# Kernel tuning notes

Measured on AMD Instinct MI355X. Metric: run time of the kernel, lower is better.

Reference implementation:

```python
import jax, jax.numpy as jnp
import numpy as np

D = 1024      # d_model
H = 16        # num_heads
DK = D // H   # head dim
L = 6         # num_layers
DFF = 4 * D   # feed-forward width
V = 32000     # vocab
B = 8         # batch
TP1 = 513     # target tokens (x length); decoded length = 512
S = 1024      # encoder frames
MAXLEN = 512
EPS = 1e-6


def make_pe(max_len, d):
    pos = np.arange(max_len, dtype=np.float64)[:, None]
    i = np.arange(0, d, 2, dtype=np.float64)[None, :]
    ang = pos / np.power(10000.0, i / d)
    pe = np.zeros((max_len, d), dtype=np.float32)
    pe[:, 0::2] = np.sin(ang)
    pe[:, 1::2] = np.cos(ang)
    return jnp.asarray(pe)


def setup_inputs() -> dict:
    key = jax.random.key(0)
    ks = jax.random.split(key, 16)
    sc = 0.02
    inp = {
        'x': jax.random.randint(ks[0], (B, TP1), 0, V, dtype=jnp.int64),
        'encoder_output': jax.random.normal(ks[1], (B, S, D), jnp.float32),
        'emb': jax.random.normal(ks[2], (V, D), jnp.float32) * sc,
        'pe': make_pe(MAXLEN, D),
        # per-layer stacked params; index 0..3 = q,k,v,out projections (in,out layout)
        'attn1_w': jax.random.normal(ks[3], (L, 4, D, D), jnp.float32) * sc,
        'attn1_b': jnp.zeros((L, 4, D), jnp.float32),
        'attn2_w': jax.random.normal(ks[4], (L, 4, D, D), jnp.float32) * sc,
        'attn2_b': jnp.zeros((L, 4, D), jnp.float32),
        'norm_a': jnp.ones((L, 3, D), jnp.float32),
        'norm_b': jnp.zeros((L, 3, D), jnp.float32),
        'ff1_w': jax.random.normal(ks[5], (L, D, DFF), jnp.float32) * sc,
        'ff1_b': jnp.zeros((L, DFF), jnp.float32),
        'ff2_w': jax.random.normal(ks[6], (L, DFF, D), jnp.float32) * sc,
        'ff2_b': jnp.zeros((L, D), jnp.float32),
        'fc_w': jax.random.normal(ks[7], (D, V), jnp.float32) * sc,
        'fc_b': jnp.zeros((V,), jnp.float32),
    }
    return inp


def _norm(x, a, b):
    mu = jnp.mean(x, axis=-1, keepdims=True)
    # torch .std() default is unbiased (ddof=1)
    var = jnp.sum((x - mu) ** 2, axis=-1, keepdims=True) / (x.shape[-1] - 1)
    return a * (x - mu) / (jnp.sqrt(var) + EPS) + b


def _mha(q_in, kv_in, w, b):
    # w: [4, D, D], b: [4, D]; masks in the original are no-ops (bug), omitted.
    bs, tq, _ = q_in.shape
    q = (q_in @ w[0] + b[0]).reshape(bs, tq, H, DK).transpose(0, 2, 1, 3)
    k = (kv_in @ w[1] + b[1]).reshape(bs, -1, H, DK).transpose(0, 2, 1, 3)
    v = (kv_in @ w[2] + b[2]).reshape(bs, -1, H, DK).transpose(0, 2, 1, 3)
    score = jnp.einsum('bhqd,bhkd->bhqk', q, k) / np.sqrt(DK).astype(np.float32)
    attn = jax.nn.softmax(score, axis=-1)
    o = jnp.einsum('bhqk,bhkd->bhqd', attn, v)
    o = o.transpose(0, 2, 1, 3).reshape(bs, tq, D)
    return o @ w[3] + b[3]


def reference(x, encoder_output, emb, pe, attn1_w, attn1_b, attn2_w, attn2_b,
              norm_a, norm_b, ff1_w, ff1_b, ff2_w, ff2_b, fc_w, fc_b):
    t = x.shape[1] - 1
    h = emb[x[:, :-1]] + pe[None, :t, :]  # [B, T, D]
    for l in range(L):
        a1 = _mha(h, h, attn1_w[l], attn1_b[l])
        h = _norm(a1 + h, norm_a[l, 0], norm_b[l, 0])
        a2 = _mha(h, encoder_output, attn2_w[l], attn2_b[l])
        h = _norm(a2 + h, norm_a[l, 1], norm_b[l, 1])
        f = jax.nn.relu(h @ ff1_w[l] + ff1_b[l]) @ ff2_w[l] + ff2_b[l]
        h = _norm(f + h, norm_a[l, 2], norm_b[l, 2])
    logits = h @ fc_w + fc_b  # [B, T, V]
    return jax.nn.log_softmax(logits, axis=-1)
```

## Files before the change

### kernel.cpp

```cpp
#include <hip/hip_runtime.h>

typedef __attribute__((ext_vector_type(4))) float f32x4;
typedef __attribute__((ext_vector_type(8))) __bf16 bfx8;
typedef unsigned short u16;
typedef unsigned int u32;

__device__ __forceinline__ u16 f2bf(float f) {
  u32 u = __builtin_bit_cast(u32, f);
  u = (u + 0x7FFFu + ((u >> 16) & 1u)) >> 16;
  return (u16)u;
}
__device__ __forceinline__ float bf2f(u16 u) {
  return __builtin_bit_cast(float, ((u32)u) << 16);
}

typedef __attribute__((address_space(1))) const void gvoid;
typedef __attribute__((address_space(3))) void svoid;
__device__ __forceinline__ void gload16(const void* g, void* l) {
  __builtin_amdgcn_global_load_lds((gvoid*)g, (svoid*)l, 16, 0, 0);
}

__device__ __forceinline__ float wredsum(float v) {
#pragma unroll
  for (int o = 32; o; o >>= 1) v += __shfl_xor(v, o, 64);
  return v;
}
__device__ __forceinline__ float wredmax(float v) {
#pragma unroll
  for (int o = 32; o; o >>= 1) v = fmaxf(v, __shfl_xor(v, o, 64));
  return v;
}

__global__ __launch_bounds__(256) void wconv_kernel(const float* __restrict__ in,
                                                    u16* __restrict__ out, int K, int N) {
  __shared__ u16 tile[32][33];
  const long z = blockIdx.z;
  const float* iz = in + z * (long)K * N;
  u16* oz = out + z * (long)K * N;
  const int n0 = blockIdx.x << 5, k0 = blockIdx.y << 5;
  const int tx = threadIdx.x & 31, ty = threadIdx.x >> 5;
#pragma unroll
  for (int i = 0; i < 4; ++i)
    tile[ty + 8 * i][tx] = f2bf(iz[(long)(k0 + ty + 8 * i) * N + n0 + tx]);
  __syncthreads();
#pragma unroll
  for (int i = 0; i < 4; ++i)
    oz[(long)(n0 + ty + 8 * i) * K + k0 + tx] = tile[tx][ty + 8 * i];
}

__global__ __launch_bounds__(256) void cvt_kernel(const float* __restrict__ in,
                                                  u16* __restrict__ out, long n) {
  long i = ((long)blockIdx.x * 256 + threadIdx.x) * 4;
  if (i + 3 < n) {
    float4 v = *(const float4*)(in + i);
    ushort4 o = {f2bf(v.x), f2bf(v.y), f2bf(v.z), f2bf(v.w)};
    *(ushort4*)(out + i) = o;
  }
}

__global__ __launch_bounds__(256) void embed_kernel(const int* __restrict__ x,
                                                    const float* __restrict__ emb,
                                                    const float* __restrict__ pe,
                                                    float* __restrict__ h,
                                                    u16* __restrict__ hb) {
  const int row = blockIdx.x;
  const int b = row >> 9, t = row & 511;
  const long tok = (long)x[b * 513 + t];
  const int d = threadIdx.x << 2;
  float4 e = *(const float4*)(emb + tok * 1024 + d);
  float4 p = *(const float4*)(pe + (long)t * 1024 + d);
  float4 v = {e.x + p.x, e.y + p.y, e.z + p.z, e.w + p.w};
  *(float4*)(h + (long)row * 1024 + d) = v;
  ushort4 o = {f2bf(v.x), f2bf(v.y), f2bf(v.z), f2bf(v.w)};
  *(ushort4*)(hb + (long)row * 1024 + d) = o;
}

__global__ __launch_bounds__(256) void addnorm_kernel(const float* __restrict__ delta,
                                                      const float* __restrict__ delta2,
                                                      float* __restrict__ h,
                                                      u16* __restrict__ hb,
                                                      const float* __restrict__ ga,
                                                      const float* __restrict__ gb) {
  __shared__ float r1[4], r2[4];
  const long row = blockIdx.x;
  const int d = threadIdx.x << 2;
  float4 a = *(const float4*)(h + row * 1024 + d);
  float4 q = *(const float4*)(delta + row * 1024 + d);
  float4 q2 = *(const float4*)(delta2 + row * 1024 + d);
  float x0 = a.x + q.x + q2.x, x1 = a.y + q.y + q2.y;
  float x2 = a.z + q.z + q2.z, x3 = a.w + q.w + q2.w;
  float s1 = wredsum(x0 + x1 + x2 + x3);
  float s2 = wredsum(x0 * x0 + x1 * x1 + x2 * x2 + x3 * x3);
  if ((threadIdx.x & 63) == 0) { r1[threadIdx.x >> 6] = s1; r2[threadIdx.x >> 6] = s2; }
  __syncthreads();
  float S1 = r1[0] + r1[1] + r1[2] + r1[3];
  float S2 = r2[0] + r2[1] + r2[2] + r2[3];
  float mu = S1 * (1.0f / 1024.0f);
  float var = (S2 - S1 * mu) * (1.0f / 1023.0f);
  float inv = 1.0f / (sqrtf(fmaxf(var, 0.f)) + 1e-6f);
  float4 g4 = *(const float4*)(ga + d);
  float4 b4 = *(const float4*)(gb + d);
  float y0 = g4.x * (x0 - mu) * inv + b4.x;
  float y1 = g4.y * (x1 - mu) * inv + b4.y;
  float y2 = g4.z * (x2 - mu) * inv + b4.z;
  float y3 = g4.w * (x3 - mu) * inv + b4.w;
  float4 y = {y0, y1, y2, y3};
  *(float4*)(h + row * 1024 + d) = y;
  ushort4 o = {f2bf(y0), f2bf(y1), f2bf(y2), f2bf(y3)};
  *(ushort4*)(hb + row * 1024 + d) = o;
}

__global__ __launch_bounds__(256) void logsoftmax_kernel(float* __restrict__ lg) {
  const long row = blockIdx.x;
  float* lr = lg + row * 32000L;
  float m = -1e30f, s = 0.f;
  for (int j = threadIdx.x; j < 8000; j += 256) {
    float4 v = *(const float4*)(lr + (long)j * 4);
    float lm = fmaxf(fmaxf(v.x, v.y), fmaxf(v.z, v.w));
    if (lm > m) { s *= __expf(m - lm); m = lm; }
    s += __expf(v.x - m) + __expf(v.y - m) + __expf(v.z - m) + __expf(v.w - m);
  }
#pragma unroll
  for (int o = 32; o; o >>= 1) {
    float om = __shfl_xor(m, o, 64), os = __shfl_xor(s, o, 64);
    float M = fmaxf(m, om);
    s = s * __expf(m - M) + os * __expf(om - M);
    m = M;
  }
  __shared__ float rm[4], rs[4];
  if ((threadIdx.x & 63) == 0) { rm[threadIdx.x >> 6] = m; rs[threadIdx.x >> 6] = s; }
  __syncthreads();
  float M = fmaxf(fmaxf(rm[0], rm[1]), fmaxf(rm[2], rm[3]));
  float S = rs[0] * __expf(rm[0] - M) + rs[1] * __expf(rm[1] - M) +
            rs[2] * __expf(rm[2] - M) + rs[3] * __expf(rm[3] - M);
  float lse = M + __logf(S);
  for (int j = threadIdx.x; j < 8000; j += 256) {
    float4 v = *(const float4*)(lr + (long)j * 4);
    v.x -= lse; v.y -= lse; v.z -= lse; v.w -= lse;
    *(float4*)(lr + (long)j * 4) = v;
  }
}

__global__ __launch_bounds__(512) void logsoftmax_bf16_kernel(const u16* __restrict__ lg,
                                                              float* __restrict__ out) {
  __shared__ u16 rl[32000];
  __shared__ float rr[8];
  const long row = blockIdx.x;
  const u16* lr = lg + row * 32000L;
  float* od = out + row * 32000L;
  const int tid = threadIdx.x;
  float m0 = -1e30f, m1 = -1e30f;
  for (int j = tid * 8; j < 32000; j += 4096) {
    ushort4 a = *(const ushort4*)(lr + j);
    ushort4 b = *(const ushort4*)(lr + j + 4);
    *(ushort4*)&rl[j] = a;
    *(ushort4*)&rl[j + 4] = b;
    m0 = fmaxf(m0, fmaxf(fmaxf(bf2f(a.x), bf2f(a.y)), fmaxf(bf2f(a.z), bf2f(a.w))));
    m1 = fmaxf(m1, fmaxf(fmaxf(bf2f(b.x), bf2f(b.y)), fmaxf(bf2f(b.z), bf2f(b.w))));
  }
  float m = wredmax(fmaxf(m0, m1));
  if ((tid & 63) == 0) rr[tid >> 6] = m;
  __syncthreads();
  m = fmaxf(fmaxf(fmaxf(rr[0], rr[1]), fmaxf(rr[2], rr[3])),
            fmaxf(fmaxf(rr[4], rr[5]), fmaxf(rr[6], rr[7])));
  __syncthreads();
  float s0 = 0.f, s1 = 0.f;
  for (int j = tid * 8; j < 32000; j += 4096) {
    ushort4 a = *(const ushort4*)&rl[j];
    ushort4 b = *(const ushort4*)&rl[j + 4];
    s0 += __expf(bf2f(a.x) - m) + __expf(bf2f(a.y) - m) +
          __expf(bf2f(a.z) - m) + __expf(bf2f(a.w) - m);
    s1 += __expf(bf2f(b.x) - m) + __expf(bf2f(b.y) - m) +
          __expf(bf2f(b.z) - m) + __expf(bf2f(b.w) - m);
  }
  float s = wredsum(s0 + s1);
  if ((tid & 63) == 0) rr[tid >> 6] = s;
  __syncthreads();
  s = rr[0] + rr[1] + rr[2] + rr[3] + rr[4] + rr[5] + rr[6] + rr[7];
  const float lse = m + __logf(s);
  for (int j = tid * 8; j < 32000; j += 4096) {
    ushort4 a = *(const ushort4*)&rl[j];
    ushort4 b = *(const ushort4*)&rl[j + 4];
    float4 o0 = {bf2f(a.x) - lse, bf2f(a.y) - lse, bf2f(a.z) - lse, bf2f(a.w) - lse};
    float4 o1 = {bf2f(b.x) - lse, bf2f(b.y) - lse, bf2f(b.z) - lse, bf2f(b.w) - lse};
    *(float4*)(od + j) = o0;
    *(float4*)(od + j + 4) = o1;
  }
}

template <int SKV>
__global__ __launch_bounds__(512) void attn_kernel(const u16* __restrict__ Q,
                                                   const u16* __restrict__ Kb,
                                                   const u16* __restrict__ Vt,
                                                   u16* __restrict__ ctx) {
  __shared__ u16 Kl[2][4096];
  __shared__ u16 Vl[2][4096];
  __shared__ u16 Pl[8][16][72];
  const int tid = threadIdx.x, lane = tid & 63, wave = tid >> 6;
  const int l15 = lane & 15, lg = lane >> 4;
  const int bh = blockIdx.y;
  const int qrow = blockIdx.x * 128 + wave * 16 + l15;
  const u16* qp = Q + ((long)bh * 512 + qrow) * 64 + lg * 8;
  bfx8 qf0 = *(const bfx8*)(qp);
  bfx8 qf1 = *(const bfx8*)(qp + 32);

  const int srow = tid >> 3;
  const int schunk = (tid & 7) ^ (srow & 7);
  const u16* Kbb = Kb + ((long)bh * SKV + srow) * 64 + schunk * 8;
  const u16* Vtb2 = Vt + ((long)bh * 64 + srow) * SKV + schunk * 8;

  auto stage = [&](int t, int buf) {
    const int kv0 = t * 64;
    gload16(Kbb + (long)kv0 * 64, &Kl[buf][tid * 8]);
    gload16(Vtb2 + kv0, &Vl[buf][tid * 8]);
  };

  const f32x4 zf = {0.f, 0.f, 0.f, 0.f};
  f32x4 acc_o[4] = {zf, zf, zf, zf};
  float mrun = -1e30f, lrun = 0.f;
  const int swk = l15 & 7;
  constexpr int NT = SKV / 64;

  stage(0, 0);
  __syncthreads();
  int buf = 0;
#pragma unroll 1
  for (int t = 0; t < NT; ++t) {
    if (t + 1 < NT) stage(t + 1, buf ^ 1);
    f32x4 sacc[4];
    __builtin_amdgcn_s_setprio(1);
#pragma unroll
    for (int kvt = 0; kvt < 4; ++kvt) {
      const int krow = kvt * 16 + l15;
      bfx8 kf0 = *(const bfx8*)&Kl[buf][krow * 64 + ((lg ^ swk) << 3)];
      bfx8 kf1 = *(const bfx8*)&Kl[buf][krow * 64 + (((4 + lg) ^ swk) << 3)];
      f32x4 tt = __builtin_amdgcn_mfma_f32_16x16x32_bf16(kf0, qf0, zf, 0, 0, 0);
      sacc[kvt] = __builtin_amdgcn_mfma_f32_16x16x32_bf16(kf1, qf1, tt, 0, 0, 0);
    }
    __builtin_amdgcn_s_setprio(0);
    float pm = -1e30f;
#pragma unroll
    for (int kvt = 0; kvt < 4; ++kvt)
#pragma unroll
      for (int r = 0; r < 4; ++r) pm = fmaxf(pm, sacc[kvt][r]);
    pm = fmaxf(pm, __shfl_xor(pm, 16, 64));
    pm = fmaxf(pm, __shfl_xor(pm, 32, 64));
    pm *= 0.125f;
    const bool grow = !__all(pm <= mrun);
    const float mnew = grow ? fmaxf(mrun, pm) : mrun;
    float psum = 0.f;
#pragma unroll
    for (int kvt = 0; kvt < 4; ++kvt)
#pragma unroll
      for (int r = 0; r < 4; ++r) {
        float p = __expf(sacc[kvt][r] * 0.125f - mnew);
        psum += p;
        Pl[wave][l15][kvt * 16 + lg * 4 + r] = f2bf(p);
      }
    psum += __shfl_xor(psum, 16, 64);
    psum += __shfl_xor(psum, 32, 64);
    if (grow) {
      const float corr = __expf(mrun - mnew);
      lrun = lrun * corr + psum;
      mrun = mnew;
#pragma unroll
      for (int dt = 0; dt < 4; ++dt) {
        acc_o[dt][0] *= corr; acc_o[dt][1] *= corr;
        acc_o[dt][2] *= corr; acc_o[dt][3] *= corr;
      }
    } else {
      lrun += psum;
    }
    bfx8 pf0 = *(const bfx8*)&Pl[wave][l15][lg * 8];
    bfx8 pf1 = *(const bfx8*)&Pl[wave][l15][32 + lg * 8];
    __builtin_amdgcn_s_setprio(1);
#pragma unroll
    for (int dt = 0; dt < 4; ++dt) {
      const int vrow = dt * 16 + l15;
      bfx8 vf0 = *(const bfx8*)&Vl[buf][vrow * 64 + ((lg ^ swk) << 3)];
      bfx8 vf1 = *(const bfx8*)&Vl[buf][vrow * 64 + (((4 + lg) ^ swk) << 3)];
      acc_o[dt] = __builtin_amdgcn_mfma_f32_16x16x32_bf16(vf0, pf0, acc_o[dt], 0, 0, 0);
      acc_o[dt] = __builtin_amdgcn_mfma_f32_16x16x32_bf16(vf1, pf1, acc_o[dt], 0, 0, 0);
    }
    __builtin_amdgcn_s_setprio(0);
    __syncthreads();
    buf ^= 1;
  }
  const float inv = 1.0f / lrun;
  const int b = bh >> 4, hh = bh & 15;
  u16* crow = ctx + ((long)b * 512 + qrow) * 1024 + hh * 64;
#pragma unroll
  for (int dt = 0; dt < 4; ++dt)
#pragma unroll
    for (int r = 0; r < 4; ++r)
      crow[dt * 16 + lg * 4 + r] = f2bf(acc_o[dt][r] * inv);
}

template <int BM, int BN, int WMW, int WNW, int EPI, bool RELU>
__global__ __launch_bounds__(256) void gemm_bt(const u16* __restrict__ A, long sAz, int lda,
                                               const u16* __restrict__ Bt, long sBz, int ldb,
                                               const float* __restrict__ bias,
                                               void* __restrict__ out, long sCz, int ldc,
                                               int K, int Ttok) {
  constexpr int WROWS = BM / WMW, WCOLS = BN / WNW;
  constexpr int MI = WROWS / 16, NI = WCOLS / 16;
  __shared__ u16 As[BM * 32];
  __shared__ u16 Bs[BN * 32];
  const int tid = threadIdx.x, lane = tid & 63, wave = tid >> 6;
  const int l15 = lane & 15, lg = lane >> 4;
  const int wm = wave / WNW, wn = wave % WNW;
  const int bx = blockIdx.x, by = blockIdx.y;
  const long z = blockIdx.z;
  const int srow = tid >> 2, scol = (tid & 3) << 3;
  const u16* Aa = A + z * sAz + (long)(by * BM + srow) * lda + scol;
  const u16* Ba = Bt + z * sBz + (long)(bx * BN + srow) * ldb + scol;

  f32x4 acc[MI][NI];
#pragma unroll
  for (int i = 0; i < MI; ++i)
#pragma unroll
    for (int j = 0; j < NI; ++j) acc[i][j] = (f32x4){0.f, 0.f, 0.f, 0.f};

  for (int kt = 0; kt < K; kt += 32) {
#pragma unroll
    for (int i = 0; i < BM / 64; ++i)
      gload16(Aa + (long)i * 64 * lda + kt, &As[i * 2048 + tid * 8]);
#pragma unroll
    for (int i = 0; i < BN / 64; ++i)
      gload16(Ba + (long)i * 64 * ldb + kt, &Bs[i * 2048 + tid * 8]);
    __syncthreads();
    bfx8 afr[MI], bfr[NI];
#pragma unroll
    for (int i = 0; i < MI; ++i)
      afr[i] = *(const bfx8*)&As[(wm * WROWS + i * 16 + l15) * 32 + (lg << 3)];
#pragma unroll
    for (int j = 0; j < NI; ++j)
      bfr[j] = *(const bfx8*)&Bs[(wn * WCOLS + j * 16 + l15) * 32 + (lg << 3)];
#pragma unroll
    for (int i = 0; i < MI; ++i)
#pragma unroll
      for (int j = 0; j < NI; ++j)
        acc[i][j] = __builtin_amdgcn_mfma_f32_16x16x32_bf16(afr[i], bfr[j], acc[i][j], 0, 0, 0);
    __syncthreads();
  }

  const int gm0 = by * BM + wm * WROWS;
  const int gn0 = bx * BN + wn * WCOLS;
#pragma unroll
  for (int i = 0; i < MI; ++i) {
#pragma unroll
    for (int j = 0; j < NI; ++j) {
      const int gn = gn0 + j * 16 + l15;
      const float bv = (bias && z == 0) ? bias[gn] : 0.f;
#pragma unroll
      for (int r = 0; r < 4; ++r) {
        const int gm = gm0 + i * 16 + (lg << 2) + r;
        float v = acc[i][j][r] + bv;
        if (RELU) v = fmaxf(v, 0.f);
        if constexpr (EPI == 0) {
          ((float*)out)[z * sCz + (long)gm * ldc + gn] = v;
        } else if constexpr (EPI == 1) {
          ((u16*)out)[z * sCz + (long)gm * ldc + gn] = f2bf(v);
        } else if constexpr (EPI == 3) {
          const int b = gm / Ttok, t = gm - b * Ttok;
          const int hh = gn >> 6, dk = gn & 63;
          ((u16*)out)[(((long)(b * 16 + hh) * Ttok + t) << 6) + dk] = f2bf(v);
        }
      }
    }
  }
}

#define MMAQ(hm, hn)                                                                   \
  {                                                                                    \
    _Pragma("unroll") for (int kk = 0; kk < 2; ++kk)                                   \
        _Pragma("unroll") for (int i = 0; i < 4; ++i)                                  \
            _Pragma("unroll") for (int jn = 0; jn < 2; ++jn)                           \
                acc[(hm)*4 + i][(hn)*2 + jn] = __builtin_amdgcn_mfma_f32_16x16x32_bf16( \
                    a[i][kk], b[jn][kk], acc[(hm)*4 + i][(hn)*2 + jn], 0, 0, 0);       \
  }

template <int EPI, bool RELU, int BMAP>
__global__ __launch_bounds__(512, 2) void gemm256(const u16* __restrict__ A, int lda,
                                                  const u16* __restrict__ Bt, int ldb,
                                                  const float* __restrict__ bias,
                                                  void* __restrict__ out, int ldc, int K,
                                                  int Ttok, void* __restrict__ out2,
                                                  void* __restrict__ out3, int gx) {
  __shared__ u16 lds[2][2][2][8192];
  const int tid = threadIdx.x, lane = tid & 63;
  const int wid = tid >> 6, wm = wid >> 2, wn = wid & 3;
  const int l15 = lane & 15, lg = lane >> 4;
  const int S = gx >> 3;
  const int xcd = blockIdx.x & 7, idx = blockIdx.x >> 3;
  const int mt = xcd * S + idx % S;
  const int nt_ = idx / S;
  const int NT = K >> 6;

  const int r0 = tid >> 3;
  const int blkx = (tid & 7) ^ (r0 & 7);
  const int n0 = nt_ * 256;
  long brow0;
  if constexpr (BMAP == 1)
    brow0 = (long)(n0 >> 11) * 4096 + 1024 + (n0 & 2047);
  else
    brow0 = n0;
  const u16* Abase = A + (long)(mt * 256 + r0) * lda + blkx * 8;
  const u16* Bbase = Bt + (brow0 + r0) * ldb + blkx * 8;

  auto stageA = [&](int s, int half) {
    const int kts = (s < NT ? s : NT - 1) << 6;
    const u16* g = Abase + (long)(half * 128) * lda + kts;
    gload16(g, &lds[s & 1][0][half][tid * 8]);
    gload16(g + (long)64 * lda, &lds[s & 1][0][half][(512 + tid) * 8]);
  };
  auto stageB = [&](int s, int half) {
    const int kts = (s < NT ? s : NT - 1) << 6;
    const u16* g = Bbase + (long)(half * 128) * ldb + kts;
    gload16(g, &lds[s & 1][1][half][tid * 8]);
    gload16(g + (long)64 * ldb, &lds[s & 1][1][half][(512 + tid) * 8]);
  };

  f32x4 acc[8][4];
#pragma unroll
  for (int i = 0; i < 8; ++i)
#pragma unroll
    for (int j = 0; j < 4; ++j) acc[i][j] = (f32x4){0.f, 0.f, 0.f, 0.f};
  bfx8 a[4][2], b[2][2];

  const int sw = l15 & 7;
  auto loadA = [&](int buf, int hm) {
#pragma unroll
    for (int i = 0; i < 4; ++i) {
      const int row = hm * 64 + i * 16 + l15;
#pragma unroll
      for (int kk = 0; kk < 2; ++kk)
        a[i][kk] = *(const bfx8*)&lds[buf][0][wm][row * 64 + (((kk * 4 + lg) ^ sw) << 3)];
    }
  };
  auto loadB = [&](int buf, int hn) {
#pragma unroll
    for (int jn = 0; jn < 2; ++jn) {
      const int row = (wn & 1) * 64 + hn * 32 + jn * 16 + l15;
#pragma unroll
      for (int kk = 0; kk < 2; ++kk)
        b[jn][kk] = *(const bfx8*)&lds[buf][1][wn >> 1][row * 64 + (((kk * 4 + lg) ^ sw) << 3)];
    }
  };

  stageA(0, 0); stageA(0, 1); stageB(0, 0); stageB(0, 1);
  stageA(1, 0); stageA(1, 1);
  asm volatile("s_waitcnt vmcnt(4)" ::: "memory");
  __builtin_amdgcn_s_barrier();

  for (int t = 0; t < NT; ++t) {
    const int p = t & 1;
    loadA(p, 0); loadB(p, 0);
    stageB(t + 1, 0);
    __builtin_amdgcn_s_barrier();
    asm volatile("s_waitcnt lgkmcnt(0)" ::: "memory");
    __builtin_amdgcn_s_setprio(1);
    MMAQ(0, 0);
    __builtin_amdgcn_s_setprio(0);
    __builtin_amdgcn_s_barrier();
    loadB(p, 1);
    stageB(t + 1, 1);
    __builtin_amdgcn_s_barrier();
    asm volatile("s_waitcnt lgkmcnt(0)" ::: "memory");
    __builtin_amdgcn_s_setprio(1);
    MMAQ(0, 1);
    __builtin_amdgcn_s_setprio(0);
    __builtin_amdgcn_s_barrier();
    loadA(p, 1); loadB(p, 0);
    stageA(t + 2, 0);
    __builtin_amdgcn_s_barrier();
    asm volatile("s_waitcnt lgkmcnt(0)" ::: "memory");
    __builtin_amdgcn_s_setprio(1);
    MMAQ(1, 0);
    __builtin_amdgcn_s_setprio(0);
    __builtin_amdgcn_s_barrier();
    loadB(p, 1);
    stageA(t + 2, 1);
    asm volatile("s_waitcnt vmcnt(4)" ::: "memory");
    __builtin_amdgcn_s_barrier();
    asm volatile("s_waitcnt lgkmcnt(0)" ::: "memory");
    __builtin_amdgcn_s_setprio(1);
    MMAQ(1, 1);
    __builtin_amdgcn_s_setprio(0);
    __builtin_amdgcn_s_barrier();
  }

  const int gm0 = mt * 256 + wm * 128;
  const int gn0 = nt_ * 256 + wn * 64;
#pragma unroll
  for (int ii = 0; ii < 8; ++ii) {
#pragma unroll
    for (int jj = 0; jj < 4; ++jj) {
      const int gn = gn0 + jj * 16 + l15;
      float bv;
      if constexpr (BMAP == 1)
        bv = bias[(gn >> 11) * 4096 + 1024 + (gn & 2047)];
      else
        bv = bias ? bias[gn] : 0.f;
#pragma unroll
      for (int r = 0; r < 4; ++r) {
        const int gm = gm0 + ii * 16 + (lg << 2) + r;
        float v = acc[ii][jj][r] + bv;
        if (RELU) v = fmaxf(v, 0.f);
        if constexpr (EPI == 0) {
          ((float*)out)[(long)gm * ldc + gn] = v;
        } else if constexpr (EPI == 1) {
          ((u16*)out)[(long)gm * ldc + gn] = f2bf(v);
        } else if constexpr (EPI == 6) {
          const int bq = gm / Ttok, t2 = gm - bq * Ttok;
          const int sec = gn >> 10, w1 = gn & 1023;
          const int hh = w1 >> 6, dk = w1 & 63;
          const u16 val = f2bf(v);
          if (sec == 0)
            ((u16*)out)[(((long)(bq * 16 + hh) * Ttok + t2) << 6) + dk] = val;
          else if (sec == 1)
            ((u16*)out2)[(((long)(bq * 16 + hh) * Ttok + t2) << 6) + dk] = val;
          else
            ((u16*)out3)[((long)((bq * 16 + hh) << 6) + dk) * Ttok + t2] = val;
        } else if constexpr (EPI == 7) {
          const int bq = gm / Ttok, t2 = gm - bq * Ttok;
          const int sec = gn >> 10, w1 = gn & 1023;
          const int hh = w1 >> 6, dk = w1 & 63;
          const u16 val = f2bf(v);
          if (sec == 0)
            ((u16*)out)[(((long)(bq * 16 + hh) * Ttok + t2) << 6) + dk] = val;
          else
            ((u16*)out2)[((long)((bq * 16 + hh) << 6) + dk) * Ttok + t2] = val;
        } else if constexpr (EPI == 8) {
          const int l = gn >> 11, inner = gn & 2047;
          const int sec = inner >> 10, w1 = inner & 1023;
          const int hh = w1 >> 6, dk = w1 & 63;
          const int bq = gm >> 10, t2 = gm & 1023;
          const u16 val = f2bf(v);
          if (sec == 0)
            ((u16*)out)[((((long)l * 8 + bq) * 16 + hh) * 1024 + t2) * 64 + dk] = val;
          else
            ((u16*)out2)[((((long)l * 8 + bq) * 16 + hh) * 64 + dk) * 1024 + t2] = val;
        }
      }
    }
  }
}

extern "C" void kernel_launch(void* const* d_in, const int* in_sizes, int n_in,
                              void* d_out, int out_size, void* d_ws, size_t ws_size,
                              hipStream_t stream) {
  const int* x = (const int*)d_in[0];
  const float* enc = (const float*)d_in[1];
  const float* emb = (const float*)d_in[2];
  const float* pe = (const float*)d_in[3];
  const float* a1w = (const float*)d_in[4];
  const float* a1b = (const float*)d_in[5];
  const float* a2w = (const float*)d_in[6];
  const float* a2b = (const float*)d_in[7];
  const float* nra = (const float*)d_in[8];
  const float* nrb = (const float*)d_in[9];
  const float* f1w = (const float*)d_in[10];
  const float* f1b = (const float*)d_in[11];
  const float* f2w = (const float*)d_in[12];
  const float* f2b = (const float*)d_in[13];
  const float* fcw = (const float*)d_in[14];
  const float* fcb = (const float*)d_in[15];
  float* out = (float*)d_out;

  char* base = (char*)d_ws;
  size_t off = 0;
  auto alloc = [&](size_t bytes) -> void* {
    void* p = base + off;
    off += (bytes + 255) & ~(size_t)255;
    return p;
  };
  const long wsz = 1024 * 1024;
  const bool big = ws_size >= (600ull << 20);
  u16* wT = (u16*)alloc(96ull * wsz * 2);
  u16* encb = (u16*)alloc(8ull * wsz * 2);
  float* h = (float*)alloc(4ull * wsz * 4);
  u16* hb = (u16*)alloc(4ull * wsz * 2);
  u16* qb = (u16*)alloc(4ull * wsz * 2);
  u16* kb = (u16*)alloc(8ull * wsz * 2);
  u16* vtb = (u16*)alloc(8ull * wsz * 2);
  u16* ctxb = (u16*)alloc(4ull * wsz * 2);
  float* af = (float*)alloc(4ull * wsz * 4);
  float* af2 = (float*)alloc(4ull * wsz * 4);
  u16* midb = (u16*)alloc(16ull * wsz * 2);
  u16* fcT = qb;
  u16* kv6 = big ? (u16*)alloc(262144000) : nullptr;
  u16* kb6 = kv6;
  u16* vtb6 = kv6 ? kv6 + 50331648 : nullptr;
  u16* lgb = kv6;

  u16* wTa1 = wT;
  u16* wTa2 = wT + 24 * wsz;
  u16* wTf1 = wT + 48 * wsz;
  u16* wTf2 = wT + 72 * wsz;

  cvt_kernel<<<dim3(8192), dim3(256), 0, stream>>>(enc, encb, 8ll * wsz);
  embed_kernel<<<dim3(4096), dim3(256), 0, stream>>>(x, emb, pe, h, hb);
  wconv_kernel<<<dim3(32, 32, 24), dim3(256), 0, stream>>>(a1w, wTa1, 1024, 1024);
  wconv_kernel<<<dim3(32, 32, 24), dim3(256), 0, stream>>>(a2w, wTa2, 1024, 1024);
  wconv_kernel<<<dim3(128, 32, 6), dim3(256), 0, stream>>>(f1w, wTf1, 1024, 4096);
  wconv_kernel<<<dim3(32, 128, 6), dim3(256), 0, stream>>>(f2w, wTf2, 4096, 1024);

  if (big) {
    gemm256<8, false, 1><<<dim3(1536), dim3(512), 0, stream>>>(
        encb, 1024, wTa2, 1024, a2b, kb6, 0, 1024, 1024, vtb6, nullptr, 32);
  }

  for (int l = 0; l < 6; ++l) {
    const float* b1 = a1b + (long)l * 4096;
    const float* b2 = a2b + (long)l * 4096;
    const u16* w1 = wTa1 + (long)l * 4 * wsz;
    const u16* w2 = wTa2 + (long)l * 4 * wsz;

    gemm256<6, false, 0><<<dim3(192), dim3(512), 0, stream>>>(
        hb, 1024, w1, 1024, b1, qb, 0, 1024, 512, kb, vtb, 16);
    attn_kernel<512><<<dim3(4, 128), dim3(512), 0, stream>>>(qb, kb, vtb, ctxb);
    gemm_bt<128, 128, 2, 2, 0, false><<<dim3(8, 32, 2), dim3(256), 0, stream>>>(
        ctxb, 512, 1024, w1 + 3 * wsz, 512, 1024, b1 + 3072, af, 4194304, 1024, 512, 0);
    addnorm_kernel<<<dim3(4096), dim3(256), 0, stream>>>(
        af, af2, h, hb, nra + (l * 3 + 0) * 1024, nrb + (l * 3 + 0) * 1024);

    gemm_bt<64, 128, 2, 2, 3, false><<<dim3(8, 64, 1), dim3(256), 0, stream>>>(
        hb, 0, 1024, w2, 0, 1024, b2, qb, 0, 0, 1024, 512);
    const u16* lK;
    const u16* lV;
    if (big) {
      lK = kb6 + (long)l * 8388608;
      lV = vtb6 + (long)l * 8388608;
    } else {
      gemm256<7, false, 0><<<dim3(256), dim3(512), 0, stream>>>(
          encb, 1024, w2 + wsz, 1024, b2 + 1024, kb, 0, 1024, 1024, vtb, nullptr, 32);
      lK = kb;
      lV = vtb;
    }
    attn_kernel<1024><<<dim3(4, 128), dim3(512), 0, stream>>>(qb, lK, lV, ctxb);
    gemm_bt<128, 128, 2, 2, 0, false><<<dim3(8, 32, 2), dim3(256), 0, stream>>>(
        ctxb, 512, 1024, w2 + 3 * wsz, 512, 1024, b2 + 3072, af, 4194304, 1024, 512, 0);
    addnorm_kernel<<<dim3(4096), dim3(256), 0, stream>>>(
        af, af2, h, hb, nra + (l * 3 + 1) * 1024, nrb + (l * 3 + 1) * 1024);

    gemm256<1, true, 0><<<dim3(256), dim3(512), 0, stream>>>(
        hb, 1024, wTf1 + (long)l * 4 * wsz, 1024, f1b + (long)l * 4096, midb, 4096, 1024, 0,
        nullptr, nullptr, 16);
    gemm_bt<128, 128, 2, 2, 0, false><<<dim3(8, 32, 2), dim3(256), 0, stream>>>(
        midb, 2048, 4096, wTf2 + (long)l * 4 * wsz, 2048, 4096, f2b + (long)l * 1024, af,
        4194304, 1024, 2048, 0);
    addnorm_kernel<<<dim3(4096), dim3(256), 0, stream>>>(
        af, af2, h, hb, nra + (l * 3 + 2) * 1024, nrb + (l * 3 + 2) * 1024);
  }

  wconv_kernel<<<dim3(1000, 32, 1), dim3(256), 0, stream>>>(fcw, fcT, 1024, 32000);
  if (big) {
    gemm256<1, false, 0><<<dim3(2000), dim3(512), 0, stream>>>(
        hb, 1024, fcT, 1024, fcb, lgb, 32000, 1024, 0, nullptr, nullptr, 16);
    logsoftmax_bf16_kernel<<<dim3(4096), dim3(512), 0, stream>>>(lgb, out);
  } else {
    gemm256<0, false, 0><<<dim3(2000), dim3(512), 0, stream>>>(
        hb, 1024, fcT, 1024, fcb, out, 32000, 1024, 0, nullptr, nullptr, 16);
    logsoftmax_kernel<<<dim3(4096), dim3(256), 0, stream>>>(out);
  }
}
```

Measured before the change: 3.031 ms.

## Store split-K partials in bf16 and split FF2 GEMM four ways

Split-K partial outputs of the output-projection and FF2 GEMMs are now written as bf16 (epilogue mode 1) into a single partial buffer instead of two fp32 buffers. The add-norm kernel is templated on the number of partials and sums them in fp32. FF2 goes from a 2-way to a 4-way K split, which raises grid parallelism. This halves the partial-sum memory traffic but rounds the partials to bf16, and the 4-way split adds one more partial read per row.

```diff
diff --git a/kernel.cpp b/kernel.cpp
--- a/kernel.cpp
+++ b/kernel.cpp
@@ -75,8 +75,8 @@
   *(ushort4*)(hb + (long)row * 1024 + d) = o;
 }
 
-__global__ __launch_bounds__(256) void addnorm_kernel(const float* __restrict__ delta,
-                                                      const float* __restrict__ delta2,
+template <int NP>
+__global__ __launch_bounds__(256) void addnorm_kernel(const u16* __restrict__ pb,
                                                       float* __restrict__ h,
                                                       u16* __restrict__ hb,
                                                       const float* __restrict__ ga,
@@ -85,10 +85,12 @@
   const long row = blockIdx.x;
   const int d = threadIdx.x << 2;
   float4 a = *(const float4*)(h + row * 1024 + d);
-  float4 q = *(const float4*)(delta + row * 1024 + d);
-  float4 q2 = *(const float4*)(delta2 + row * 1024 + d);
-  float x0 = a.x + q.x + q2.x, x1 = a.y + q.y + q2.y;
-  float x2 = a.z + q.z + q2.z, x3 = a.w + q.w + q2.w;
+  float x0 = a.x, x1 = a.y, x2 = a.z, x3 = a.w;
+#pragma unroll
+  for (int n = 0; n < NP; ++n) {
+    ushort4 q = *(const ushort4*)(pb + (long)n * 4194304 + row * 1024 + d);
+    x0 += bf2f(q.x); x1 += bf2f(q.y); x2 += bf2f(q.z); x3 += bf2f(q.w);
+  }
   float s1 = wredsum(x0 + x1 + x2 + x3);
   float s2 = wredsum(x0 * x0 + x1 * x1 + x2 * x2 + x3 * x3);
   if ((threadIdx.x & 63) == 0) { r1[threadIdx.x >> 6] = s1; r2[threadIdx.x >> 6] = s2; }
@@ -585,8 +587,7 @@
   u16* kb = (u16*)alloc(8ull * wsz * 2);
   u16* vtb = (u16*)alloc(8ull * wsz * 2);
   u16* ctxb = (u16*)alloc(4ull * wsz * 2);
-  float* af = (float*)alloc(4ull * wsz * 4);
-  float* af2 = (float*)alloc(4ull * wsz * 4);
+  u16* pb = (u16*)alloc(16ull * wsz * 2);
   u16* midb = (u16*)alloc(16ull * wsz * 2);
   u16* fcT = qb;
   u16* kv6 = big ? (u16*)alloc(262144000) : nullptr;
@@ -620,10 +621,10 @@
     gemm256<6, false, 0><<<dim3(192), dim3(512), 0, stream>>>(
         hb, 1024, w1, 1024, b1, qb, 0, 1024, 512, kb, vtb, 16);
     attn_kernel<512><<<dim3(4, 128), dim3(512), 0, stream>>>(qb, kb, vtb, ctxb);
-    gemm_bt<128, 128, 2, 2, 0, false><<<dim3(8, 32, 2), dim3(256), 0, stream>>>(
-        ctxb, 512, 1024, w1 + 3 * wsz, 512, 1024, b1 + 3072, af, 4194304, 1024, 512, 0);
-    addnorm_kernel<<<dim3(4096), dim3(256), 0, stream>>>(
-        af, af2, h, hb, nra + (l * 3 + 0) * 1024, nrb + (l * 3 + 0) * 1024);
+    gemm_bt<128, 128, 2, 2, 1, false><<<dim3(8, 32, 2), dim3(256), 0, stream>>>(
+        ctxb, 512, 1024, w1 + 3 * wsz, 512, 1024, b1 + 3072, pb, 4194304, 1024, 512, 0);
+    addnorm_kernel<2><<<dim3(4096), dim3(256), 0, stream>>>(
+        pb, h, hb, nra + (l * 3 + 0) * 1024, nrb + (l * 3 + 0) * 1024);
 
     gemm_bt<64, 128, 2, 2, 3, false><<<dim3(8, 64, 1), dim3(256), 0, stream>>>(
         hb, 0, 1024, w2, 0, 1024, b2, qb, 0, 0, 1024, 512);
@@ -639,19 +640,19 @@
       lV = vtb;
     }
     attn_kernel<1024><<<dim3(4, 128), dim3(512), 0, stream>>>(qb, lK, lV, ctxb);
-    gemm_bt<128, 128, 2, 2, 0, false><<<dim3(8, 32, 2), dim3(256), 0, stream>>>(
-        ctxb, 512, 1024, w2 + 3 * wsz, 512, 1024, b2 + 3072, af, 4194304, 1024, 512, 0);
-    addnorm_kernel<<<dim3(4096), dim3(256), 0, stream>>>(
-        af, af2, h, hb, nra + (l * 3 + 1) * 1024, nrb + (l * 3 + 1) * 1024);
+    gemm_bt<128, 128, 2, 2, 1, false><<<dim3(8, 32, 2), dim3(256), 0, stream>>>(
+        ctxb, 512, 1024, w2 + 3 * wsz, 512, 1024, b2 + 3072, pb, 4194304, 1024, 512, 0);
+    addnorm_kernel<2><<<dim3(4096), dim3(256), 0, stream>>>(
+        pb, h, hb, nra + (l * 3 + 1) * 1024, nrb + (l * 3 + 1) * 1024);
 
     gemm256<1, true, 0><<<dim3(256), dim3(512), 0, stream>>>(
         hb, 1024, wTf1 + (long)l * 4 * wsz, 1024, f1b + (long)l * 4096, midb, 4096, 1024, 0,
         nullptr, nullptr, 16);
-    gemm_bt<128, 128, 2, 2, 0, false><<<dim3(8, 32, 2), dim3(256), 0, stream>>>(
-        midb, 2048, 4096, wTf2 + (long)l * 4 * wsz, 2048, 4096, f2b + (long)l * 1024, af,
-        4194304, 1024, 2048, 0);
-    addnorm_kernel<<<dim3(4096), dim3(256), 0, stream>>>(
-        af, af2, h, hb, nra + (l * 3 + 2) * 1024, nrb + (l * 3 + 2) * 1024);
+    gemm_bt<128, 128, 2, 2, 1, false><<<dim3(8, 32, 4), dim3(256), 0, stream>>>(
+        midb, 1024, 4096, wTf2 + (long)l * 4 * wsz, 1024, 4096, f2b + (long)l * 1024, pb,
+        4194304, 1024, 1024, 0);
+    addnorm_kernel<4><<<dim3(4096), dim3(256), 0, stream>>>(
+        pb, h, hb, nra + (l * 3 + 2) * 1024, nrb + (l * 3 + 2) * 1024);
   }
 
   wconv_kernel<<<dim3(1000, 32, 1), dim3(256), 0, stream>>>(fcw, fcT, 1024, 32000);
```

New measurement: 3.035 ms. About the same (+0.2%).
